# Kernel tuning notes

Hardware: AMD Instinct MI355X
Metric: run time of the kernel (lower is better)

## Reference

```python
import jax, jax.numpy as jnp
import numpy as np

NEG_SLOPE = 0.01


def _forward(data_meteo, data_hydro, hydro_edge_index, meteo_edge_index,
             W_rel_m, b_rel_m, W_root_m, W_rel_h, b_rel_h, W_root_h,
             W_ih, W_hh, b_ih, b_hh, W_lin, b_lin):
    B, T, Nh, Fh = data_hydro.shape
    Nm, Fm = data_meteo.shape[2], data_meteo.shape[3]
    G = B * T  # independent graphs (one per batch element per timestep)
    xh = data_hydro.reshape(G, Nh, Fh)
    xm = data_meteo.reshape(G, Nm, Fm)

    src_h, tgt_h = hydro_edge_index[0], hydro_edge_index[1]
    src_m, tgt_m = meteo_edge_index[0], meteo_edge_index[1]

    # GraphConv (hydro -> hydro): sum-aggregate neighbors, then lin_rel + lin_root
    agg_h = jnp.zeros((G, Nh, Fh), xh.dtype).at[:, tgt_h].add(xh[:, src_h])
    out_h = agg_h @ W_rel_h.T + b_rel_h + xh @ W_root_h.T

    # GraphConv (meteo -> hydro)
    agg_m = jnp.zeros((G, Nh, Fm), xm.dtype).at[:, tgt_m].add(xm[:, src_m])
    out_m = agg_m @ W_rel_m.T + b_rel_m + xh @ W_root_m.T

    # HeteroConv aggr='mean' over the two edge types targeting hydro nodes
    x = jax.nn.leaky_relu(0.5 * (out_h + out_m), NEG_SLOPE)  # [G, Nh, Hg]
    Hg = x.shape[-1]
    x = x.reshape(B, T, Nh, Hg).transpose(1, 0, 2, 3)  # [T, B, Nh, Hg]

    # Batched per-node LSTM (PyTorch gate order i, f, g, o)
    Hl = W_hh.shape[-1]
    bias = b_ih + b_hh  # [Nh, 4*Hl]

    def step(carry, x_t):
        h, c = carry
        gates = (jnp.einsum('bnf,ngf->bng', x_t, W_ih)
                 + jnp.einsum('bnh,ngh->bng', h, W_hh) + bias)
        i, f, g, o = jnp.split(gates, 4, axis=-1)
        c = jax.nn.sigmoid(f) * c + jax.nn.sigmoid(i) * jnp.tanh(g)
        h = jax.nn.sigmoid(o) * jnp.tanh(c)
        return (h, c), None

    h0 = jnp.zeros((B, Nh, Hl), x.dtype)
    (h_last, _), _ = jax.lax.scan(step, (h0, h0), x)

    pred = h_last @ W_lin.T + b_lin  # [B, Nh, futurelen]
    return jax.nn.leaky_relu(pred, NEG_SLOPE)


def setup_inputs() -> dict:
    key = jax.random.key(0)
    ks = jax.random.split(key, 12)
    B, T, Nh, Nm = 32, 336, 100, 150
    Fh, Fm, Hg, Hl, FUT = 8, 16, 64, 64, 24
    Eh, Em = 300, 500
    s = 0.1
    return {
        'data_meteo': jax.random.normal(ks[0], (B, T, Nm, Fm), jnp.float32),
        'data_hydro': jax.random.normal(ks[1], (B, T, Nh, Fh), jnp.float32),
        'hydro_edge_index': jax.random.randint(ks[2], (2, Eh), 0, Nh, jnp.int32),
        'meteo_edge_index': jax.random.randint(ks[3], (2, Em), 0, Nh, jnp.int32),
        'W_rel_m': jax.random.normal(ks[4], (Hg, Fm), jnp.float32) * s,
        'b_rel_m': jnp.zeros((Hg,), jnp.float32),
        'W_root_m': jax.random.normal(ks[5], (Hg, Fh), jnp.float32) * s,
        'W_rel_h': jax.random.normal(ks[6], (Hg, Fh), jnp.float32) * s,
        'b_rel_h': jnp.zeros((Hg,), jnp.float32),
        'W_root_h': jax.random.normal(ks[7], (Hg, Fh), jnp.float32) * s,
        'W_ih': jax.random.normal(ks[8], (Nh, 4 * Hl, Hg), jnp.float32) * s,
        'W_hh': jax.random.normal(ks[9], (Nh, 4 * Hl, Hl), jnp.float32) * s,
        'b_ih': jnp.zeros((Nh, 4 * Hl), jnp.float32),
        'b_hh': jnp.zeros((Nh, 4 * Hl), jnp.float32),
        'W_lin': jax.random.normal(ks[10], (FUT, Hl), jnp.float32) * s,
        'b_lin': jnp.zeros((FUT,), jnp.float32),
    }


def reference(data_meteo, data_hydro, hydro_edge_index, meteo_edge_index,
              W_rel_m, b_rel_m, W_root_m, W_rel_h, b_rel_h, W_root_h,
              W_ih, W_hh, b_ih, b_hh, W_lin, b_lin):
    return _forward(data_meteo, data_hydro, hydro_edge_index, meteo_edge_index,
                    W_rel_m, b_rel_m, W_root_m, W_rel_h, b_rel_h, W_root_h,
                    W_ih, W_hh, b_ih, b_hh, W_lin, b_lin)
```

## Files before the change

kernel.cpp:

```cpp
#include <hip/hip_runtime.h>
#include <hip/hip_fp16.h>

#define B_ 32
#define T_ 336
#define NH 100
#define NM 150
#define FH 8
#define FM 16
#define HG 64
#define FUT 24
#define EH 300
#define EM 500

#define WRELH 0
#define WRELM 512
#define WROOT 1536
#define BIASC 2048
#define OFFH  2112
#define SRCH  2304
#define OFFM  2624
#define SRCM  2752
#define XBUF_F 4096

typedef _Float16 half8 __attribute__((ext_vector_type(8)));
typedef float floatx4 __attribute__((ext_vector_type(4)));

#define XH_STRIDE 136
#define GSTRIDE   266

__device__ __forceinline__ float fsigmoid(float x) {
    return __builtin_amdgcn_rcpf(1.0f + __expf(-x));
}
__device__ __forceinline__ float ftanh(float x) {
    return 1.0f - 2.0f * __builtin_amdgcn_rcpf(1.0f + __expf(2.0f * x));
}
__device__ __forceinline__ float lrelu(float x) { return x >= 0.0f ? x : 0.01f * x; }

__global__ __launch_bounds__(256) void prep_kernel(
    const float* __restrict__ W_rel_m, const float* __restrict__ b_rel_m,
    const float* __restrict__ W_root_m, const float* __restrict__ W_rel_h,
    const float* __restrict__ b_rel_h, const float* __restrict__ W_root_h,
    const int* __restrict__ he, const int* __restrict__ me,
    float* __restrict__ ws)
{
    const int tid = threadIdx.x;
    int* wsI = (int*)ws;
    __shared__ int cnt[NH + 1];
    __shared__ int cur[NH + 1];

    for (int idx = tid; idx < HG * FH; idx += 256) {
        int j = idx >> 3, k = idx & 7;
        ws[WRELH + k * HG + j] = 0.5f * W_rel_h[j * FH + k];
        ws[WROOT + k * HG + j] = 0.5f * (W_root_h[j * FH + k] + W_root_m[j * FH + k]);
    }
    for (int idx = tid; idx < HG * FM; idx += 256) {
        int j = idx >> 4, k = idx & 15;
        ws[WRELM + k * HG + j] = 0.5f * W_rel_m[j * FM + k];
    }
    if (tid < HG) ws[BIASC + tid] = 0.5f * (b_rel_h[tid] + b_rel_m[tid]);

    if (tid <= NH) cnt[tid] = 0;
    __syncthreads();
    for (int e = tid; e < EH; e += 256) atomicAdd(&cnt[he[EH + e]], 1);
    __syncthreads();
    if (tid == 0) {
        int s = 0;
        for (int n2 = 0; n2 < NH; ++n2) { int c = cnt[n2]; cur[n2] = s; cnt[n2] = s; s += c; }
        cnt[NH] = s;
    }
    __syncthreads();
    if (tid <= NH) wsI[OFFH + tid] = cnt[tid];
    for (int e = tid; e < EH; e += 256) {
        int t = he[EH + e];
        int p = atomicAdd(&cur[t], 1);
        wsI[SRCH + p] = he[e];
    }
    __syncthreads();

    if (tid <= NH) cnt[tid] = 0;
    __syncthreads();
    for (int e = tid; e < EM; e += 256) atomicAdd(&cnt[me[EM + e]], 1);
    __syncthreads();
    if (tid == 0) {
        int s = 0;
        for (int n2 = 0; n2 < NH; ++n2) { int c = cnt[n2]; cur[n2] = s; cnt[n2] = s; s += c; }
        cnt[NH] = s;
    }
    __syncthreads();
    if (tid <= NH) wsI[OFFM + tid] = cnt[tid];
    for (int e = tid; e < EM; e += 256) {
        int t = me[EM + e];
        int p = atomicAdd(&cur[t], 1);
        wsI[SRCM + p] = me[e];
    }
}

__global__ __launch_bounds__(256) void gnn_kernel(
    const float* __restrict__ dm, const float* __restrict__ dh,
    const float* __restrict__ ws, __half* __restrict__ xout)
{
    __shared__ __align__(16) float xh[NH * FH];
    __shared__ __align__(16) float xm[NM * FM];
    __shared__ __align__(16) float aggh[NH * FH];
    __shared__ __align__(16) float aggm[NH * FM];
    __shared__ __align__(16) float wrelh[FH * HG];
    __shared__ __align__(16) float wrelm[FM * HG];
    __shared__ __align__(16) float wroot[FH * HG];
    __shared__ __align__(16) float biasc[HG];
    __shared__ int offh[NH + 1], offm[NH + 1];
    __shared__ int srch[EH], srcm[EM];

    const int tid = threadIdx.x;
    const int g = blockIdx.x;
    const int* wsI = (const int*)ws;

    {
        const float4* s = (const float4*)(dh + (size_t)g * (NH * FH));
        for (int i = tid; i < (NH * FH) / 4; i += 256) ((float4*)xh)[i] = s[i];
    }
    {
        const float4* s = (const float4*)(dm + (size_t)g * (NM * FM));
        for (int i = tid; i < (NM * FM) / 4; i += 256) ((float4*)xm)[i] = s[i];
    }
    for (int i = tid; i < (FH * HG) / 4; i += 256) {
        ((float4*)wrelh)[i] = ((const float4*)(ws + WRELH))[i];
        ((float4*)wroot)[i] = ((const float4*)(ws + WROOT))[i];
    }
    for (int i = tid; i < (FM * HG) / 4; i += 256)
        ((float4*)wrelm)[i] = ((const float4*)(ws + WRELM))[i];
    if (tid < HG) biasc[tid] = ws[BIASC + tid];
    for (int i = tid; i <= NH; i += 256) { offh[i] = wsI[OFFH + i]; offm[i] = wsI[OFFM + i]; }
    for (int i = tid; i < EH; i += 256) srch[i] = wsI[SRCH + i];
    for (int i = tid; i < EM; i += 256) srcm[i] = wsI[SRCM + i];
    __syncthreads();

    for (int s = tid; s < NH * FH; s += 256) {
        int n = s >> 3, k = s & 7;
        float a = 0.f;
        for (int e = offh[n]; e < offh[n + 1]; ++e) a += xh[srch[e] * FH + k];
        aggh[s] = a;
    }
    for (int s = tid; s < NH * FM; s += 256) {
        int n = s >> 4, k = s & 15;
        float a = 0.f;
        for (int e = offm[n]; e < offm[n + 1]; ++e) a += xm[srcm[e] * FM + k];
        aggm[s] = a;
    }
    __syncthreads();

    __half* xg = xout + (size_t)g * (NH * HG);
    for (int task = tid; task < NH * 16; task += 256) {
        int n = task >> 4;
        int j0 = (task & 15) << 2;
        float4 acc = *(const float4*)&biasc[j0];
#pragma unroll
        for (int k = 0; k < FH; ++k) {
            float a = aggh[n * FH + k];
            float4 w = *(const float4*)&wrelh[k * HG + j0];
            acc.x += a * w.x; acc.y += a * w.y; acc.z += a * w.z; acc.w += a * w.w;
        }
#pragma unroll
        for (int k = 0; k < FM; ++k) {
            float a = aggm[n * FM + k];
            float4 w = *(const float4*)&wrelm[k * HG + j0];
            acc.x += a * w.x; acc.y += a * w.y; acc.z += a * w.z; acc.w += a * w.w;
        }
#pragma unroll
        for (int k = 0; k < FH; ++k) {
            float a = xh[n * FH + k];
            float4 w = *(const float4*)&wroot[k * HG + j0];
            acc.x += a * w.x; acc.y += a * w.y; acc.z += a * w.z; acc.w += a * w.w;
        }
        acc.x = lrelu(acc.x); acc.y = lrelu(acc.y); acc.z = lrelu(acc.z); acc.w = lrelu(acc.w);
        __half2 lo = __halves2half2(__float2half_rn(acc.x), __float2half_rn(acc.y));
        __half2 hi = __halves2half2(__float2half_rn(acc.z), __float2half_rn(acc.w));
        *(__half2*)(xg + n * HG + j0) = lo;
        *(__half2*)(xg + n * HG + j0 + 2) = hi;
    }
}

__global__ __launch_bounds__(512) void lstm_kernel(
    const __half* __restrict__ xbuf,
    const float* __restrict__ Wih, const float* __restrict__ Whh,
    const float* __restrict__ bih, const float* __restrict__ bhh,
    const float* __restrict__ Wlin, const float* __restrict__ blin,
    float* __restrict__ out)
{
    __shared__ __align__(16) _Float16 xh[16 * XH_STRIDE];
    __shared__ __align__(16) float gates[16 * GSTRIDE];
    __shared__ __align__(16) float hb32[16 * 68];

    const int tid = threadIdx.x;
    const int n = blockIdx.x >> 1;
    const int half_ = blockIdx.x & 1;
    const int w = tid >> 6, l = tid & 63;
    const int m16 = l & 15, g4 = l >> 4;

    half8 bf[2][4];
    float biasr[2];
#pragma unroll
    for (int gti = 0; gti < 2; ++gti) {
        const int gcol = 32 * w + 16 * gti + m16;
        const float* wi = Wih + ((size_t)n * 256 + gcol) * 64;
        const float* wh = Whh + ((size_t)n * 256 + gcol) * 64;
        biasr[gti] = bih[n * 256 + gcol] + bhh[n * 256 + gcol];
#pragma unroll
        for (int kt = 0; kt < 4; ++kt) {
            const int kb = kt * 32 + g4 * 8;
            const float* src = (kb < 64) ? (wi + kb) : (wh + (kb - 64));
            float4 lo = *(const float4*)src;
            float4 hi = *(const float4*)(src + 4);
            half8 f;
            f[0] = (_Float16)lo.x; f[1] = (_Float16)lo.y;
            f[2] = (_Float16)lo.z; f[3] = (_Float16)lo.w;
            f[4] = (_Float16)hi.x; f[5] = (_Float16)hi.y;
            f[6] = (_Float16)hi.z; f[7] = (_Float16)hi.w;
            bf[gti][kt] = f;
        }
    }
    const float bias0 = biasr[0], bias1 = biasr[1];

    const unsigned short* xb_u = (const unsigned short*)xbuf;
    const int pb = tid >> 4;
    const int pk = (tid & 15) << 2;
    const size_t xrowbase = (size_t)(half_ * 16 + pb) * T_ * (NH * HG) + (size_t)n * HG + pk;

    const int cu = tid & 63;
    const int cb0 = (tid >> 6) * 2, cb1 = cb0 + 1;

    if (tid < 256) {
        ushort4 x0 = *(const ushort4*)(xb_u + xrowbase);
        *(ushort4*)((unsigned short*)xh + pb * XH_STRIDE + pk) = x0;
    }
    for (int i = tid; i < 16 * 64; i += 512)
        xh[(i >> 6) * XH_STRIDE + 64 + (i & 63)] = (_Float16)0.f;
    __syncthreads();

    float cc0 = 0.f, cc1 = 0.f;
    ushort4 xpre;

#pragma unroll 1
    for (int t = 0; t < T_; ++t) {
        if (tid < 256) {
            const int tn = (t + 1 < T_) ? (t + 1) : (T_ - 1);
            xpre = *(const ushort4*)(xb_u + xrowbase + (size_t)tn * (NH * HG));
        }
        half8 af[4];
#pragma unroll
        for (int kt = 0; kt < 4; ++kt)
            af[kt] = *(const half8*)&xh[m16 * XH_STRIDE + kt * 32 + g4 * 8];

        floatx4 c0 = {bias0, bias0, bias0, bias0};
        floatx4 c1 = {bias1, bias1, bias1, bias1};
#pragma unroll
        for (int kt = 0; kt < 4; ++kt) {
            c0 = __builtin_amdgcn_mfma_f32_16x16x32_f16(af[kt], bf[0][kt], c0, 0, 0, 0);
            c1 = __builtin_amdgcn_mfma_f32_16x16x32_f16(af[kt], bf[1][kt], c1, 0, 0, 0);
        }
#pragma unroll
        for (int r = 0; r < 4; ++r) {
            gates[(4 * g4 + r) * GSTRIDE + 32 * w + m16]      = c0[r];
            gates[(4 * g4 + r) * GSTRIDE + 32 * w + 16 + m16] = c1[r];
        }
        __syncthreads();

        {
            float gi = gates[cb0 * GSTRIDE + cu];
            float gf = gates[cb0 * GSTRIDE + 64 + cu];
            float gg = gates[cb0 * GSTRIDE + 128 + cu];
            float go = gates[cb0 * GSTRIDE + 192 + cu];
            cc0 = fsigmoid(gf) * cc0 + fsigmoid(gi) * ftanh(gg);
            float h0 = fsigmoid(go) * ftanh(cc0);

            float gi1 = gates[cb1 * GSTRIDE + cu];
            float gf1 = gates[cb1 * GSTRIDE + 64 + cu];
            float gg1 = gates[cb1 * GSTRIDE + 128 + cu];
            float go1 = gates[cb1 * GSTRIDE + 192 + cu];
            cc1 = fsigmoid(gf1) * cc1 + fsigmoid(gi1) * ftanh(gg1);
            float h1 = fsigmoid(go1) * ftanh(cc1);

            xh[cb0 * XH_STRIDE + 64 + cu] = (_Float16)h0;
            xh[cb1 * XH_STRIDE + 64 + cu] = (_Float16)h1;
            if (t == T_ - 1) { hb32[cb0 * 68 + cu] = h0; hb32[cb1 * 68 + cu] = h1; }
        }
        if (tid < 256)
            *(ushort4*)((unsigned short*)xh + pb * XH_STRIDE + pk) = xpre;
        __syncthreads();
    }

    if (tid < 16 * FUT) {
        int b = tid / FUT, j = tid - b * FUT;
        float acc = blin[j];
        const float* wl = Wlin + j * 64;
        const float* hr = &hb32[b * 68];
#pragma unroll
        for (int k = 0; k < 64; k += 4) {
            float4 wv = *(const float4*)&wl[k];
            acc += wv.x * hr[k] + wv.y * hr[k + 1] + wv.z * hr[k + 2] + wv.w * hr[k + 3];
        }
        out[((size_t)(half_ * 16 + b) * NH + n) * FUT + j] = lrelu(acc);
    }
}

extern "C" void kernel_launch(void* const* d_in, const int* in_sizes, int n_in,
                              void* d_out, int out_size, void* d_ws, size_t ws_size,
                              hipStream_t stream)
{
    const float* dm       = (const float*)d_in[0];
    const float* dh       = (const float*)d_in[1];
    const int*   he       = (const int*)d_in[2];
    const int*   me       = (const int*)d_in[3];
    const float* W_rel_m  = (const float*)d_in[4];
    const float* b_rel_m  = (const float*)d_in[5];
    const float* W_root_m = (const float*)d_in[6];
    const float* W_rel_h  = (const float*)d_in[7];
    const float* b_rel_h  = (const float*)d_in[8];
    const float* W_root_h = (const float*)d_in[9];
    const float* Wih      = (const float*)d_in[10];
    const float* Whh      = (const float*)d_in[11];
    const float* bih      = (const float*)d_in[12];
    const float* bhh      = (const float*)d_in[13];
    const float* Wlin     = (const float*)d_in[14];
    const float* blin     = (const float*)d_in[15];

    float* ws = (float*)d_ws;
    __half* xbuf = (__half*)(ws + XBUF_F);
    float* out = (float*)d_out;

    prep_kernel<<<1, 256, 0, stream>>>(W_rel_m, b_rel_m, W_root_m,
                                       W_rel_h, b_rel_h, W_root_h, he, me, ws);
    gnn_kernel<<<B_ * T_, 256, 0, stream>>>(dm, dh, ws, xbuf);
    lstm_kernel<<<NH * 2, 512, 0, stream>>>(xbuf, Wih, Whh, bih, bhh, Wlin, blin, out);
}
```

Measured before the change: 583.2 us.

## Fuse LSTM gate math into MFMA lanes with double-buffered state, batch GNN graphs

The LSTM kernel now has each wave compute all four gates for its 16 hidden units, so the cell update runs directly on the MFMA accumulators. This removes the shared gates buffer and one of the two barriers per timestep, and a double-buffered x/h tile lets the next step's input be written without a race. The block shrinks from 512 to 256 threads, which doubles the MFMAs per wave. The GNN kernel processes two graphs per block, concatenates the aggregated and root features so one 32x64 weight matrix serves a single register-tiled matmul, and reuses the weight and edge loads across both graphs.

Measured after the change: 846.1 us. +45.1%, slower.

```diff
diff --git a/kernel.cpp b/kernel.cpp
--- a/kernel.cpp
+++ b/kernel.cpp
@@ -26,7 +26,7 @@
 typedef float floatx4 __attribute__((ext_vector_type(4)));
 
 #define XH_STRIDE 136
-#define GSTRIDE   266
+#define GPB 2
 
 __device__ __forceinline__ float fsigmoid(float x) {
     return __builtin_amdgcn_rcpf(1.0f + __expf(-x));
@@ -101,93 +101,101 @@
 {
     __shared__ __align__(16) float xh[NH * FH];
     __shared__ __align__(16) float xm[NM * FM];
-    __shared__ __align__(16) float aggh[NH * FH];
-    __shared__ __align__(16) float aggm[NH * FM];
-    __shared__ __align__(16) float wrelh[FH * HG];
-    __shared__ __align__(16) float wrelm[FM * HG];
-    __shared__ __align__(16) float wroot[FH * HG];
+    __shared__ __align__(16) float vcat[NH * 36];
+    __shared__ __align__(16) float wcat[32 * 64];
     __shared__ __align__(16) float biasc[HG];
     __shared__ int offh[NH + 1], offm[NH + 1];
     __shared__ int srch[EH], srcm[EM];
 
     const int tid = threadIdx.x;
-    const int g = blockIdx.x;
     const int* wsI = (const int*)ws;
 
-    {
-        const float4* s = (const float4*)(dh + (size_t)g * (NH * FH));
-        for (int i = tid; i < (NH * FH) / 4; i += 256) ((float4*)xh)[i] = s[i];
-    }
-    {
-        const float4* s = (const float4*)(dm + (size_t)g * (NM * FM));
-        for (int i = tid; i < (NM * FM) / 4; i += 256) ((float4*)xm)[i] = s[i];
-    }
-    for (int i = tid; i < (FH * HG) / 4; i += 256) {
-        ((float4*)wrelh)[i] = ((const float4*)(ws + WRELH))[i];
-        ((float4*)wroot)[i] = ((const float4*)(ws + WROOT))[i];
-    }
-    for (int i = tid; i < (FM * HG) / 4; i += 256)
-        ((float4*)wrelm)[i] = ((const float4*)(ws + WRELM))[i];
+    for (int i = tid; i < 2048 / 4; i += 256) ((float4*)wcat)[i] = ((const float4*)ws)[i];
     if (tid < HG) biasc[tid] = ws[BIASC + tid];
     for (int i = tid; i <= NH; i += 256) { offh[i] = wsI[OFFH + i]; offm[i] = wsI[OFFM + i]; }
     for (int i = tid; i < EH; i += 256) srch[i] = wsI[SRCH + i];
     for (int i = tid; i < EM; i += 256) srcm[i] = wsI[SRCM + i];
-    __syncthreads();
-
-    for (int s = tid; s < NH * FH; s += 256) {
-        int n = s >> 3, k = s & 7;
-        float a = 0.f;
-        for (int e = offh[n]; e < offh[n + 1]; ++e) a += xh[srch[e] * FH + k];
-        aggh[s] = a;
-    }
-    for (int s = tid; s < NH * FM; s += 256) {
-        int n = s >> 4, k = s & 15;
-        float a = 0.f;
-        for (int e = offm[n]; e < offm[n + 1]; ++e) a += xm[srcm[e] * FM + k];
-        aggm[s] = a;
-    }
-    __syncthreads();
-
-    __half* xg = xout + (size_t)g * (NH * HG);
-    for (int task = tid; task < NH * 16; task += 256) {
-        int n = task >> 4;
-        int j0 = (task & 15) << 2;
-        float4 acc = *(const float4*)&biasc[j0];
-#pragma unroll
-        for (int k = 0; k < FH; ++k) {
-            float a = aggh[n * FH + k];
-            float4 w = *(const float4*)&wrelh[k * HG + j0];
-            acc.x += a * w.x; acc.y += a * w.y; acc.z += a * w.z; acc.w += a * w.w;
-        }
-#pragma unroll
-        for (int k = 0; k < FM; ++k) {
-            float a = aggm[n * FM + k];
-            float4 w = *(const float4*)&wrelm[k * HG + j0];
-            acc.x += a * w.x; acc.y += a * w.y; acc.z += a * w.z; acc.w += a * w.w;
-        }
-#pragma unroll
-        for (int k = 0; k < FH; ++k) {
-            float a = xh[n * FH + k];
-            float4 w = *(const float4*)&wroot[k * HG + j0];
-            acc.x += a * w.x; acc.y += a * w.y; acc.z += a * w.z; acc.w += a * w.w;
-        }
-        acc.x = lrelu(acc.x); acc.y = lrelu(acc.y); acc.z = lrelu(acc.z); acc.w = lrelu(acc.w);
-        __half2 lo = __halves2half2(__float2half_rn(acc.x), __float2half_rn(acc.y));
-        __half2 hi = __halves2half2(__float2half_rn(acc.z), __float2half_rn(acc.w));
-        *(__half2*)(xg + n * HG + j0) = lo;
-        *(__half2*)(xg + n * HG + j0 + 2) = hi;
-    }
-}
-
-__global__ __launch_bounds__(512) void lstm_kernel(
+
+    const int r  = tid >> 4;
+    const int j0 = (tid & 15) << 2;
+    const int cnt_n = (r < 4) ? 7 : 6;
+
+#pragma unroll 1
+    for (int gi = 0; gi < GPB; ++gi) {
+        const int g = blockIdx.x * GPB + gi;
+        {
+            const float4* s = (const float4*)(dh + (size_t)g * (NH * FH));
+            for (int i = tid; i < (NH * FH) / 4; i += 256) ((float4*)xh)[i] = s[i];
+        }
+        {
+            const float4* s = (const float4*)(dm + (size_t)g * (NM * FM));
+            for (int i = tid; i < (NM * FM) / 4; i += 256) ((float4*)xm)[i] = s[i];
+        }
+        __syncthreads();
+
+        for (int s = tid; s < NH * FH; s += 256) {
+            int nn = s >> 3, k = s & 7;
+            float a = 0.f;
+            for (int e = offh[nn]; e < offh[nn + 1]; ++e) a += xh[srch[e] * FH + k];
+            vcat[nn * 36 + k] = a;
+            vcat[nn * 36 + 24 + k] = xh[nn * FH + k];
+        }
+        for (int s = tid; s < NH * FM; s += 256) {
+            int nn = s >> 4, k = s & 15;
+            float a = 0.f;
+            for (int e = offm[nn]; e < offm[nn + 1]; ++e) a += xm[srcm[e] * FM + k];
+            vcat[nn * 36 + 8 + k] = a;
+        }
+        __syncthreads();
+
+        float4 acc[7];
+        const float4 bias4 = *(const float4*)&biasc[j0];
+#pragma unroll
+        for (int i = 0; i < 7; ++i) acc[i] = bias4;
+
+#pragma unroll
+        for (int k4 = 0; k4 < 8; ++k4) {
+            float4 w0 = *(const float4*)&wcat[(4 * k4 + 0) * 64 + j0];
+            float4 w1 = *(const float4*)&wcat[(4 * k4 + 1) * 64 + j0];
+            float4 w2 = *(const float4*)&wcat[(4 * k4 + 2) * 64 + j0];
+            float4 w3 = *(const float4*)&wcat[(4 * k4 + 3) * 64 + j0];
+#pragma unroll
+            for (int i = 0; i < 7; ++i) {
+                if (i < cnt_n) {
+                    int nn = r + 16 * i;
+                    float4 va = *(const float4*)&vcat[nn * 36 + 4 * k4];
+                    acc[i].x += va.x * w0.x + va.y * w1.x + va.z * w2.x + va.w * w3.x;
+                    acc[i].y += va.x * w0.y + va.y * w1.y + va.z * w2.y + va.w * w3.y;
+                    acc[i].z += va.x * w0.z + va.y * w1.z + va.z * w2.z + va.w * w3.z;
+                    acc[i].w += va.x * w0.w + va.y * w1.w + va.z * w2.w + va.w * w3.w;
+                }
+            }
+        }
+
+        __half* xg = xout + (size_t)g * (NH * HG);
+#pragma unroll
+        for (int i = 0; i < 7; ++i) {
+            if (i < cnt_n) {
+                int nn = r + 16 * i;
+                float ax = lrelu(acc[i].x), ay = lrelu(acc[i].y);
+                float az = lrelu(acc[i].z), aw = lrelu(acc[i].w);
+                __half2 lo = __halves2half2(__float2half_rn(ax), __float2half_rn(ay));
+                __half2 hi = __halves2half2(__float2half_rn(az), __float2half_rn(aw));
+                __half2* dst = (__half2*)(xg + nn * HG + j0);
+                dst[0] = lo; dst[1] = hi;
+            }
+        }
+    }
+}
+
+__global__ __launch_bounds__(256) void lstm_kernel(
     const __half* __restrict__ xbuf,
     const float* __restrict__ Wih, const float* __restrict__ Whh,
     const float* __restrict__ bih, const float* __restrict__ bhh,
     const float* __restrict__ Wlin, const float* __restrict__ blin,
     float* __restrict__ out)
 {
-    __shared__ __align__(16) _Float16 xh[16 * XH_STRIDE];
-    __shared__ __align__(16) float gates[16 * GSTRIDE];
+    __shared__ __align__(16) _Float16 xh2[2][16 * XH_STRIDE];
     __shared__ __align__(16) float hb32[16 * 68];
 
     const int tid = threadIdx.x;
@@ -195,15 +203,16 @@
     const int half_ = blockIdx.x & 1;
     const int w = tid >> 6, l = tid & 63;
     const int m16 = l & 15, g4 = l >> 4;
-
-    half8 bf[2][4];
-    float biasr[2];
-#pragma unroll
-    for (int gti = 0; gti < 2; ++gti) {
-        const int gcol = 32 * w + 16 * gti + m16;
+    const int u = 16 * w + m16;
+
+    half8 bf[4][4];
+    float biasr[4];
+#pragma unroll
+    for (int g = 0; g < 4; ++g) {
+        const int gcol = 64 * g + u;
         const float* wi = Wih + ((size_t)n * 256 + gcol) * 64;
         const float* wh = Whh + ((size_t)n * 256 + gcol) * 64;
-        biasr[gti] = bih[n * 256 + gcol] + bhh[n * 256 + gcol];
+        biasr[g] = bih[n * 256 + gcol] + bhh[n * 256 + gcol];
 #pragma unroll
         for (int kt = 0; kt < 4; ++kt) {
             const int kb = kt * 32 + g4 * 8;
@@ -215,90 +224,79 @@
             f[2] = (_Float16)lo.z; f[3] = (_Float16)lo.w;
             f[4] = (_Float16)hi.x; f[5] = (_Float16)hi.y;
             f[6] = (_Float16)hi.z; f[7] = (_Float16)hi.w;
-            bf[gti][kt] = f;
-        }
-    }
-    const float bias0 = biasr[0], bias1 = biasr[1];
+            bf[g][kt] = f;
+        }
+    }
 
     const unsigned short* xb_u = (const unsigned short*)xbuf;
     const int pb = tid >> 4;
     const int pk = (tid & 15) << 2;
     const size_t xrowbase = (size_t)(half_ * 16 + pb) * T_ * (NH * HG) + (size_t)n * HG + pk;
 
-    const int cu = tid & 63;
-    const int cb0 = (tid >> 6) * 2, cb1 = cb0 + 1;
-
-    if (tid < 256) {
+    {
         ushort4 x0 = *(const ushort4*)(xb_u + xrowbase);
-        *(ushort4*)((unsigned short*)xh + pb * XH_STRIDE + pk) = x0;
-    }
-    for (int i = tid; i < 16 * 64; i += 512)
-        xh[(i >> 6) * XH_STRIDE + 64 + (i & 63)] = (_Float16)0.f;
-    __syncthreads();
-
-    float cc0 = 0.f, cc1 = 0.f;
-    ushort4 xpre;
+        *(ushort4*)((unsigned short*)&xh2[0][0] + pb * XH_STRIDE + pk) = x0;
+    }
+    for (int i = tid; i < 16 * 64; i += 256)
+        xh2[0][(i >> 6) * XH_STRIDE + 64 + (i & 63)] = (_Float16)0.f;
+    __syncthreads();
+
+    float cc[4] = {0.f, 0.f, 0.f, 0.f};
+    int p = 0;
 
 #pragma unroll 1
     for (int t = 0; t < T_; ++t) {
-        if (tid < 256) {
-            const int tn = (t + 1 < T_) ? (t + 1) : (T_ - 1);
-            xpre = *(const ushort4*)(xb_u + xrowbase + (size_t)tn * (NH * HG));
-        }
+        const int tn = (t + 1 < T_) ? (t + 1) : (T_ - 1);
+        ushort4 xpre = *(const ushort4*)(xb_u + xrowbase + (size_t)tn * (NH * HG));
+
+        const _Float16* cb = &xh2[p][0];
         half8 af[4];
 #pragma unroll
         for (int kt = 0; kt < 4; ++kt)
-            af[kt] = *(const half8*)&xh[m16 * XH_STRIDE + kt * 32 + g4 * 8];
-
-        floatx4 c0 = {bias0, bias0, bias0, bias0};
-        floatx4 c1 = {bias1, bias1, bias1, bias1};
+            af[kt] = *(const half8*)&cb[m16 * XH_STRIDE + kt * 32 + g4 * 8];
+
+        floatx4 acc[4];
+#pragma unroll
+        for (int g = 0; g < 4; ++g) {
+            float bg = biasr[g];
+            floatx4 c = {bg, bg, bg, bg};
+            acc[g] = c;
+        }
 #pragma unroll
         for (int kt = 0; kt < 4; ++kt) {
-            c0 = __builtin_amdgcn_mfma_f32_16x16x32_f16(af[kt], bf[0][kt], c0, 0, 0, 0);
-            c1 = __builtin_amdgcn_mfma_f32_16x16x32_f16(af[kt], bf[1][kt], c1, 0, 0, 0);
-        }
+#pragma unroll
+            for (int g = 0; g < 4; ++g)
+                acc[g] = __builtin_amdgcn_mfma_f32_16x16x32_f16(af[kt], bf[g][kt], acc[g], 0, 0, 0);
+        }
+
+        _Float16* nb = &xh2[p ^ 1][0];
 #pragma unroll
         for (int r = 0; r < 4; ++r) {
-            gates[(4 * g4 + r) * GSTRIDE + 32 * w + m16]      = c0[r];
-            gates[(4 * g4 + r) * GSTRIDE + 32 * w + 16 + m16] = c1[r];
-        }
+            const int bb = 4 * g4 + r;
+            float ai = acc[0][r], afv = acc[1][r], ag = acc[2][r], ao = acc[3][r];
+            float c = fsigmoid(afv) * cc[r] + fsigmoid(ai) * ftanh(ag);
+            cc[r] = c;
+            float h = fsigmoid(ao) * ftanh(c);
+            nb[bb * XH_STRIDE + 64 + u] = (_Float16)h;
+            if (t == T_ - 1) hb32[bb * 68 + u] = h;
+        }
+        *(ushort4*)((unsigned short*)nb + pb * XH_STRIDE + pk) = xpre;
+
         __syncthreads();
-
-        {
-            float gi = gates[cb0 * GSTRIDE + cu];
-            float gf = gates[cb0 * GSTRIDE + 64 + cu];
-            float gg = gates[cb0 * GSTRIDE + 128 + cu];
-            float go = gates[cb0 * GSTRIDE + 192 + cu];
-            cc0 = fsigmoid(gf) * cc0 + fsigmoid(gi) * ftanh(gg);
-            float h0 = fsigmoid(go) * ftanh(cc0);
-
-            float gi1 = gates[cb1 * GSTRIDE + cu];
-            float gf1 = gates[cb1 * GSTRIDE + 64 + cu];
-            float gg1 = gates[cb1 * GSTRIDE + 128 + cu];
-            float go1 = gates[cb1 * GSTRIDE + 192 + cu];
-            cc1 = fsigmoid(gf1) * cc1 + fsigmoid(gi1) * ftanh(gg1);
-            float h1 = fsigmoid(go1) * ftanh(cc1);
-
-            xh[cb0 * XH_STRIDE + 64 + cu] = (_Float16)h0;
-            xh[cb1 * XH_STRIDE + 64 + cu] = (_Float16)h1;
-            if (t == T_ - 1) { hb32[cb0 * 68 + cu] = h0; hb32[cb1 * 68 + cu] = h1; }
-        }
-        if (tid < 256)
-            *(ushort4*)((unsigned short*)xh + pb * XH_STRIDE + pk) = xpre;
-        __syncthreads();
-    }
-
-    if (tid < 16 * FUT) {
-        int b = tid / FUT, j = tid - b * FUT;
-        float acc = blin[j];
+        p ^= 1;
+    }
+
+    for (int task = tid; task < 16 * FUT; task += 256) {
+        int b = task / FUT, j = task - b * FUT;
+        float accv = blin[j];
         const float* wl = Wlin + j * 64;
         const float* hr = &hb32[b * 68];
 #pragma unroll
         for (int k = 0; k < 64; k += 4) {
             float4 wv = *(const float4*)&wl[k];
-            acc += wv.x * hr[k] + wv.y * hr[k + 1] + wv.z * hr[k + 2] + wv.w * hr[k + 3];
-        }
-        out[((size_t)(half_ * 16 + b) * NH + n) * FUT + j] = lrelu(acc);
+            accv += wv.x * hr[k] + wv.y * hr[k + 1] + wv.z * hr[k + 2] + wv.w * hr[k + 3];
+        }
+        out[((size_t)(half_ * 16 + b) * NH + n) * FUT + j] = lrelu(accv);
     }
 }
 
@@ -329,6 +327,6 @@
 
     prep_kernel<<<1, 256, 0, stream>>>(W_rel_m, b_rel_m, W_root_m,
                                        W_rel_h, b_rel_h, W_root_h, he, me, ws);
-    gnn_kernel<<<B_ * T_, 256, 0, stream>>>(dm, dh, ws, xbuf);
-    lstm_kernel<<<NH * 2, 512, 0, stream>>>(xbuf, Wih, Whh, bih, bhh, Wlin, blin, out);
-}
+    gnn_kernel<<<(B_ * T_) / GPB, 256, 0, stream>>>(dm, dh, ws, xbuf);
+    lstm_kernel<<<NH * 2, 256, 0, stream>>>(xbuf, Wih, Whh, bih, bhh, Wlin, blin, out);
+}
```
